# Performance work log

Hardware: AMD Instinct MI355X
Metric: run time of the kernel (lower is better)

Reference implementation:

```python
import jax, jax.numpy as jnp
import numpy as np

NUM_HEADS = 12


def setup_inputs() -> dict:
    key = jax.random.key(0)
    k1, k2, k3 = jax.random.split(key, 3)
    B, S, E = 1, 4096, 768
    x = jax.random.normal(k1, (B, S, E), dtype=jnp.float32)
    # learned parameters (nn.Linear weights, stored as [in, out] for x @ W)
    w_qkv = jax.random.normal(k2, (E, 3 * E), dtype=jnp.float32) * 0.02
    b_qkv = jnp.zeros((3 * E,), dtype=jnp.float32)
    w_out = jax.random.normal(k3, (E, E), dtype=jnp.float32) * 0.02
    b_out = jnp.zeros((E,), dtype=jnp.float32)
    return {"x": x, "w_qkv": w_qkv, "b_qkv": b_qkv, "w_out": w_out, "b_out": b_out}


def reference(x, w_qkv, b_qkv, w_out, b_out):
    """Single-process (world_size==1) path of the module:
    qkv projection -> multi-head scaled-dot-product softmax attention
    (non-causal) -> output projection. Dropout is identity in eval.
    """
    B, S, E = x.shape
    H = NUM_HEADS
    D = E // H
    scale = 1.0 / jnp.sqrt(jnp.asarray(D, dtype=x.dtype))

    qkv = x @ w_qkv + b_qkv                       # [B, S, 3E]
    qkv = qkv.reshape(B, S, 3, H, D)
    qkv = jnp.transpose(qkv, (2, 0, 3, 1, 4))     # [3, B, H, S, D]
    q, k, v = qkv[0], qkv[1], qkv[2]

    scores = jnp.einsum("bhqd,bhkd->bhqk", q * scale, k)  # [B, H, S, S]
    attn = jax.nn.softmax(scores, axis=-1)
    out = jnp.einsum("bhqk,bhkd->bhqd", attn, v)           # [B, H, S, D]

    out = jnp.transpose(out, (0, 2, 1, 3)).reshape(B, S, E)
    return out @ w_out + b_out
```

## Files before the change

kernel.cpp:

```cpp
#include <hip/hip_runtime.h>

typedef __attribute__((ext_vector_type(8))) short bh8;
typedef __attribute__((ext_vector_type(4))) float fx4;

__device__ __forceinline__ unsigned short f2bf(float f) {
    unsigned int u = __float_as_uint(f);
    u += 0x7FFF + ((u >> 16) & 1);
    return (unsigned short)(u >> 16);
}

__device__ __forceinline__ unsigned int cvtpk_bf16(float a, float b) {
    unsigned int r;
    asm("v_cvt_pk_bf16_f32 %0, %1, %2" : "=v"(r) : "v"(a), "v"(b));
    return r;
}

__device__ __forceinline__ bh8 pack4(unsigned int a, unsigned int b,
                                     unsigned int c, unsigned int d) {
    union { unsigned int u[4]; bh8 h; } z;
    z.u[0] = a; z.u[1] = b; z.u[2] = c; z.u[3] = d;
    return z.h;
}

__device__ __forceinline__ void stage_rows8(const unsigned short* g, long ldg,
                                            unsigned short* lds, int lane) {
    int r8 = lane >> 3;
    int gc = (lane & 7) ^ r8;
    __builtin_amdgcn_global_load_lds(
        (const __attribute__((address_space(1))) void*)(g + (long)r8 * ldg + gc * 8),
        (__attribute__((address_space(3))) void*)lds, 16, 0, 0);
}

__device__ __forceinline__ bh8 frag_ld(const unsigned short* t, int row, int kchunk, int lane) {
    int ch = (kchunk + (lane >> 4)) ^ (row & 7);
    return *(const bh8*)(t + row * 64 + ch * 8);
}

__global__ __launch_bounds__(256) void castbf(const float* __restrict__ x,
                                              unsigned short* __restrict__ y, int n) {
    int i = (blockIdx.x * 256 + threadIdx.x) * 4;
    if (i < n) {
        float4 v = *(const float4*)(x + i);
        ushort4 o = make_ushort4(f2bf(v.x), f2bf(v.y), f2bf(v.z), f2bf(v.w));
        *(ushort4*)(y + i) = o;
    }
}

__global__ __launch_bounds__(256) void transW(const float* __restrict__ W,
                                              unsigned short* __restrict__ Wt,
                                              int K, int N) {
    __shared__ float t[32][33];
    const int n0 = blockIdx.x * 32, k0 = blockIdx.y * 32;
    const int tx = threadIdx.x & 31, ty = threadIdx.x >> 5;
    #pragma unroll
    for (int r = ty; r < 32; r += 8)
        t[r][tx] = W[(size_t)(k0 + r) * N + n0 + tx];
    __syncthreads();
    #pragma unroll
    for (int r = ty; r < 32; r += 8)
        Wt[(size_t)(n0 + r) * K + k0 + tx] = f2bf(t[tx][r]);
}

__global__ __launch_bounds__(256) void gemm_qkv(const unsigned short* __restrict__ A,
                                                const unsigned short* __restrict__ Bt,
                                                const float* __restrict__ bias,
                                                unsigned short* __restrict__ Cout,
                                                unsigned short* __restrict__ vt) {
    const int M = 4096, N = 2304, K = 768;
    __shared__ __align__(16) char smem[49152];
    unsigned short* Ash0 = (unsigned short*)smem;
    unsigned short* Ash1 = (unsigned short*)(smem + 8192);
    unsigned short* Bsh0 = (unsigned short*)(smem + 16384);
    unsigned short* Bsh1 = (unsigned short*)(smem + 32768);
    unsigned short* Tsc  = (unsigned short*)smem;

    const int m0 = blockIdx.y * 64, n0 = blockIdx.x * 128;
    const int tid = threadIdx.x, wid = tid >> 6, lane = tid & 63;
    const int wr = (wid >> 1) * 32, wc = (wid & 1) * 64;

    #pragma unroll
    for (int g = 0; g < 2; ++g) {
        int rt = (wid * 2 + g) * 8;
        stage_rows8(A + (size_t)(m0 + rt) * K, K, Ash0 + rt * 64, lane);
    }
    #pragma unroll
    for (int g = 0; g < 4; ++g) {
        int rt = (wid * 4 + g) * 8;
        stage_rows8(Bt + (size_t)(n0 + rt) * K, K, Bsh0 + rt * 64, lane);
    }
    __syncthreads();

    fx4 acc[2][4];
    #pragma unroll
    for (int i = 0; i < 2; ++i)
        #pragma unroll
        for (int j = 0; j < 4; ++j)
            acc[i][j] = (fx4){0.f, 0.f, 0.f, 0.f};

    int kn = 64;
    auto kstep = [&](const unsigned short* Ac, const unsigned short* Bc,
                     unsigned short* Ad, unsigned short* Bd, bool pref) {
        if (pref) {
            #pragma unroll
            for (int g = 0; g < 2; ++g) {
                int rt = (wid * 2 + g) * 8;
                stage_rows8(A + (size_t)(m0 + rt) * K + kn, K, Ad + rt * 64, lane);
            }
            #pragma unroll
            for (int g = 0; g < 4; ++g) {
                int rt = (wid * 4 + g) * 8;
                stage_rows8(Bt + (size_t)(n0 + rt) * K + kn, K, Bd + rt * 64, lane);
            }
            kn += 64;
        }
        #pragma unroll
        for (int ks = 0; ks < 2; ++ks) {
            bh8 af[2], bfr[4];
            #pragma unroll
            for (int i = 0; i < 2; ++i) af[i] = frag_ld(Ac, wr + i * 16 + (lane & 15), ks * 4, lane);
            #pragma unroll
            for (int j = 0; j < 4; ++j) bfr[j] = frag_ld(Bc, wc + j * 16 + (lane & 15), ks * 4, lane);
            #pragma unroll
            for (int i = 0; i < 2; ++i)
                #pragma unroll
                for (int j = 0; j < 4; ++j)
                    acc[i][j] = __builtin_amdgcn_mfma_f32_16x16x32_bf16(af[i], bfr[j], acc[i][j], 0, 0, 0);
        }
        __syncthreads();
    };

    for (int t2 = 0; t2 < 6; ++t2) {
        kstep(Ash0, Bsh0, Ash1, Bsh1, true);
        kstep(Ash1, Bsh1, Ash0, Bsh0, t2 < 5);
    }

    const int cc = lane & 15, g4 = (lane >> 4) * 4;
    if (n0 < 1536) {
        #pragma unroll
        for (int j = 0; j < 4; ++j) {
            int col = n0 + wc + j * 16 + cc;
            float bv = bias[col];
            float sc = (col < 768) ? 0.18033688011112042f : 1.0f;
            #pragma unroll
            for (int i = 0; i < 2; ++i) {
                #pragma unroll
                for (int r = 0; r < 4; ++r) {
                    int row = m0 + wr + i * 16 + g4 + r;
                    Cout[(size_t)row * N + col] = f2bf((acc[i][j][r] + bv) * sc);
                }
            }
        }
    } else {
        #pragma unroll
        for (int j = 0; j < 4; ++j) {
            int dloc = wc + j * 16 + cc;
            float bv = bias[n0 + dloc];
            #pragma unroll
            for (int i = 0; i < 2; ++i) {
                int sloc = wr + i * 16 + g4;
                unsigned int u0 = cvtpk_bf16(acc[i][j][0] + bv, acc[i][j][1] + bv);
                unsigned int u1 = cvtpk_bf16(acc[i][j][2] + bv, acc[i][j][3] + bv);
                *(uint2*)(Tsc + dloc * 68 + sloc) = make_uint2(u0, u1);
            }
        }
        __syncthreads();
        const int d = tid >> 1, hf = (tid & 1) << 5;
        const unsigned short* srow = Tsc + d * 68;
        unsigned short* dst = vt + (size_t)(n0 - 1536 + d) * 4096 + m0 + hf;
        #pragma unroll
        for (int k = 0; k < 4; ++k) {
            int y = hf + 8 * k;
            int sb = (y & 32) + ((y & 24) >> 1);
            uint2 lo = *(const uint2*)(srow + sb);
            uint2 hi = *(const uint2*)(srow + sb + 16);
            *(uint4*)(dst + 8 * k) = make_uint4(lo.x, lo.y, hi.x, hi.y);
        }
    }
}

__global__ __launch_bounds__(256) void gemm64(const unsigned short* __restrict__ A,
                                              const unsigned short* __restrict__ Bt,
                                              const float* __restrict__ bias,
                                              float* __restrict__ Cout,
                                              int M, int N, int K) {
    __shared__ __align__(16) unsigned short Ash[2][64 * 64];
    __shared__ __align__(16) unsigned short Bsh[2][64 * 64];
    const int m0 = blockIdx.y * 64, n0 = blockIdx.x * 64;
    const int tid = threadIdx.x, wid = tid >> 6, lane = tid & 63;
    const int wr = (wid >> 1) * 32, wc = (wid & 1) * 32;

    #pragma unroll
    for (int g = 0; g < 2; ++g) {
        int rt = (wid * 2 + g) * 8;
        stage_rows8(A + (size_t)(m0 + rt) * K, K, Ash[0] + rt * 64, lane);
        stage_rows8(Bt + (size_t)(n0 + rt) * K, K, Bsh[0] + rt * 64, lane);
    }
    __syncthreads();

    fx4 acc[2][2];
    #pragma unroll
    for (int i = 0; i < 2; ++i)
        #pragma unroll
        for (int j = 0; j < 2; ++j)
            acc[i][j] = (fx4){0.f, 0.f, 0.f, 0.f};

    int kn = 64;
    auto kstep = [&](const unsigned short* Ac, const unsigned short* Bc,
                     unsigned short* Ad, unsigned short* Bd, bool pref) {
        if (pref) {
            #pragma unroll
            for (int g = 0; g < 2; ++g) {
                int rt = (wid * 2 + g) * 8;
                stage_rows8(A + (size_t)(m0 + rt) * K + kn, K, Ad + rt * 64, lane);
                stage_rows8(Bt + (size_t)(n0 + rt) * K + kn, K, Bd + rt * 64, lane);
            }
            kn += 64;
        }
        #pragma unroll
        for (int ks = 0; ks < 2; ++ks) {
            bh8 af[2], bfr[2];
            #pragma unroll
            for (int i = 0; i < 2; ++i) af[i] = frag_ld(Ac, wr + i * 16 + (lane & 15), ks * 4, lane);
            #pragma unroll
            for (int j = 0; j < 2; ++j) bfr[j] = frag_ld(Bc, wc + j * 16 + (lane & 15), ks * 4, lane);
            #pragma unroll
            for (int i = 0; i < 2; ++i)
                #pragma unroll
                for (int j = 0; j < 2; ++j)
                    acc[i][j] = __builtin_amdgcn_mfma_f32_16x16x32_bf16(af[i], bfr[j], acc[i][j], 0, 0, 0);
        }
        __syncthreads();
    };

    for (int t2 = 0; t2 < 6; ++t2) {
        kstep(Ash[0], Bsh[0], Ash[1], Bsh[1], true);
        kstep(Ash[1], Bsh[1], Ash[0], Bsh[0], t2 < 5);
    }

    const int cc = lane & 15, g4 = (lane >> 4) * 4;
    #pragma unroll
    for (int j = 0; j < 2; ++j) {
        int col = n0 + wc + j * 16 + cc;
        float bv = bias[col];
        #pragma unroll
        for (int i = 0; i < 2; ++i) {
            #pragma unroll
            for (int r = 0; r < 4; ++r) {
                int row = m0 + wr + i * 16 + g4 + r;
                Cout[(size_t)row * N + col] = acc[i][j][r] + bv;
            }
        }
    }
}

__global__ __launch_bounds__(256) void attn_fwd(const unsigned short* __restrict__ qkv,
                                                const unsigned short* __restrict__ vt,
                                                unsigned short* __restrict__ ao) {
    __shared__ __align__(16) char smem[40960];
    unsigned short* Qs  = (unsigned short*)smem;
    unsigned short* Ks0 = (unsigned short*)(smem + 8192);
    unsigned short* Ks1 = (unsigned short*)(smem + 16384);
    unsigned short* Vs0 = (unsigned short*)(smem + 24576);
    unsigned short* Vs1 = (unsigned short*)(smem + 32768);
    float* Of    = (float*)smem;
    float* l_lds = (float*)(smem + 17408);

    const int h = blockIdx.y, q0 = blockIdx.x * 64;
    const int tid = threadIdx.x, wid = tid >> 6, lane = tid & 63;
    const int g = lane >> 4, qc = lane & 15, x = qc & 7;
    const int wq = wid >> 1, wk = wid & 1;

    const unsigned short* qg_ = qkv + (size_t)q0 * 2304 + h * 64;
    const unsigned short* kgb = qkv + 768 + h * 64;
    const unsigned short* vgb = vt + (size_t)h * 64 * 4096;

    #pragma unroll
    for (int gg = 0; gg < 2; ++gg) {
        int rt = (wid * 2 + gg) * 8;
        stage_rows8(qg_ + (size_t)rt * 2304, 2304, Qs + rt * 64, lane);
        stage_rows8(kgb + (size_t)rt * 2304, 2304, Ks0 + rt * 64, lane);
        stage_rows8(vgb + (size_t)rt * 4096, 4096, Vs0 + rt * 64, lane);
    }
    __syncthreads();

    bh8 qf[2][2];
    #pragma unroll
    for (int qg = 0; qg < 2; ++qg)
        #pragma unroll
        for (int kc = 0; kc < 2; ++kc)
            qf[qg][kc] = frag_ld(Qs, 32 * wq + 16 * qg + qc, 4 * kc, lane);

    int koff[2][2], voff[4];
    #pragma unroll
    for (int jm = 0; jm < 2; ++jm)
        #pragma unroll
        for (int kc = 0; kc < 2; ++kc)
            koff[jm][kc] = (32 * wk + 16 * jm + qc) * 64 + ((4 * kc + g) ^ x) * 8;
    #pragma unroll
    for (int dj = 0; dj < 4; ++dj)
        voff[dj] = (16 * dj + qc) * 64 + ((4 * wk + g) ^ x) * 8;

    float lrun[2] = {0.f, 0.f};
    fx4 oacP[4][2];
    #pragma unroll
    for (int dj = 0; dj < 4; ++dj)
        #pragma unroll
        for (int qg = 0; qg < 2; ++qg)
            oacP[dj][qg] = (fx4){0.f, 0.f, 0.f, 0.f};

    const unsigned short* knext = kgb + (size_t)64 * 2304;
    const unsigned short* vnext = vgb + 64;

    auto tile_step = [&](const unsigned short* Kc, const unsigned short* Vc,
                         unsigned short* Kd, unsigned short* Vd, bool pref) {
        if (pref) {
            #pragma unroll
            for (int gg = 0; gg < 2; ++gg) {
                int rt = (wid * 2 + gg) * 8;
                stage_rows8(knext + (size_t)rt * 2304, 2304, Kd + rt * 64, lane);
                stage_rows8(vnext + (size_t)rt * 4096, 4096, Vd + rt * 64, lane);
            }
            knext += (size_t)64 * 2304;
            vnext += 64;
        }

        bh8 kf[2][2];
        #pragma unroll
        for (int jm = 0; jm < 2; ++jm) {
            kf[jm][0] = *(const bh8*)(Kc + koff[jm][0]);
            kf[jm][1] = *(const bh8*)(Kc + koff[jm][1]);
        }
        fx4 sT[2][2];
        __builtin_amdgcn_s_setprio(1);
        #pragma unroll
        for (int jm = 0; jm < 2; ++jm)
            #pragma unroll
            for (int qg = 0; qg < 2; ++qg) {
                fx4 z = (fx4){0.f, 0.f, 0.f, 0.f};
                z = __builtin_amdgcn_mfma_f32_16x16x32_bf16(kf[jm][0], qf[qg][0], z, 0, 0, 0);
                z = __builtin_amdgcn_mfma_f32_16x16x32_bf16(kf[jm][1], qf[qg][1], z, 0, 0, 0);
                sT[jm][qg] = z;
            }
        __builtin_amdgcn_s_setprio(0);

        #pragma unroll
        for (int jm = 0; jm < 2; ++jm)
            #pragma unroll
            for (int qg = 0; qg < 2; ++qg) {
                sT[jm][qg][0] = __builtin_amdgcn_exp2f(sT[jm][qg][0]);
                sT[jm][qg][1] = __builtin_amdgcn_exp2f(sT[jm][qg][1]);
                sT[jm][qg][2] = __builtin_amdgcn_exp2f(sT[jm][qg][2]);
                sT[jm][qg][3] = __builtin_amdgcn_exp2f(sT[jm][qg][3]);
                lrun[qg] += (sT[jm][qg][0] + sT[jm][qg][1]) + (sT[jm][qg][2] + sT[jm][qg][3]);
            }

        bh8 vf[4];
        #pragma unroll
        for (int dj = 0; dj < 4; ++dj) vf[dj] = *(const bh8*)(Vc + voff[dj]);
        __builtin_amdgcn_s_setprio(1);
        #pragma unroll
        for (int qg = 0; qg < 2; ++qg) {
            bh8 pb = pack4(cvtpk_bf16(sT[0][qg][0], sT[0][qg][1]),
                           cvtpk_bf16(sT[0][qg][2], sT[0][qg][3]),
                           cvtpk_bf16(sT[1][qg][0], sT[1][qg][1]),
                           cvtpk_bf16(sT[1][qg][2], sT[1][qg][3]));
            #pragma unroll
            for (int dj = 0; dj < 4; ++dj)
                oacP[dj][qg] = __builtin_amdgcn_mfma_f32_16x16x32_bf16(vf[dj], pb, oacP[dj][qg], 0, 0, 0);
        }
        __builtin_amdgcn_s_setprio(0);
        __syncthreads();
    };

    for (int t2 = 0; t2 < 32; ++t2) {
        tile_step(Ks0, Vs0, Ks1, Vs1, true);
        tile_step(Ks1, Vs1, Ks0, Vs0, t2 < 31);
    }

    #pragma unroll
    for (int qg = 0; qg < 2; ++qg) {
        lrun[qg] += __shfl_xor(lrun[qg], 16);
        lrun[qg] += __shfl_xor(lrun[qg], 32);
    }
    if (wk == 1) {
        #pragma unroll
        for (int qg = 0; qg < 2; ++qg) {
            int q = 32 * wq + 16 * qg + qc;
            #pragma unroll
            for (int dj = 0; dj < 4; ++dj)
                *(fx4*)(Of + q * 68 + 16 * dj + 4 * g) = oacP[dj][qg];
            l_lds[q] = lrun[qg];
        }
    }
    __syncthreads();
    if (wk == 0) {
        #pragma unroll
        for (int qg = 0; qg < 2; ++qg) {
            int q = 32 * wq + 16 * qg + qc;
            float inv = 1.0f / (lrun[qg] + l_lds[q]);
            unsigned short* aop = ao + (size_t)(q0 + q) * 768 + h * 64;
            #pragma unroll
            for (int dj = 0; dj < 4; ++dj) {
                fx4 o = oacP[dj][qg];
                fx4 p = *(const fx4*)(Of + q * 68 + 16 * dj + 4 * g);
                int d0 = dj * 16 + 4 * g;
                *(unsigned int*)(aop + d0)     = cvtpk_bf16((o[0] + p[0]) * inv, (o[1] + p[1]) * inv);
                *(unsigned int*)(aop + d0 + 2) = cvtpk_bf16((o[2] + p[2]) * inv, (o[3] + p[3]) * inv);
            }
        }
    }
}

extern "C" void kernel_launch(void* const* d_in, const int* in_sizes, int n_in,
                              void* d_out, int out_size, void* d_ws, size_t ws_size,
                              hipStream_t stream) {
    const float* x     = (const float*)d_in[0];
    const float* w_qkv = (const float*)d_in[1];
    const float* b_qkv = (const float*)d_in[2];
    const float* w_out = (const float*)d_in[3];
    const float* b_out = (const float*)d_in[4];
    float* out = (float*)d_out;

    const int S = 4096, E = 768, E3 = 2304, H = 12;

    unsigned short* xb    = (unsigned short*)d_ws;
    unsigned short* wqkvT = xb    + (size_t)S * E;
    unsigned short* woutT = wqkvT + (size_t)E3 * E;
    unsigned short* qkvb  = woutT + (size_t)E * E;
    unsigned short* vtp   = qkvb  + (size_t)S * E3;
    unsigned short* ao    = vtp   + (size_t)H * 64 * S;

    castbf<<<dim3((S * E) / (256 * 4)), 256, 0, stream>>>(x, xb, S * E);
    transW<<<dim3(E3 / 32, E / 32), 256, 0, stream>>>(w_qkv, wqkvT, E, E3);
    transW<<<dim3(E / 32, E / 32), 256, 0, stream>>>(w_out, woutT, E, E);
    gemm_qkv<<<dim3(E3 / 128, S / 64), 256, 0, stream>>>(xb, wqkvT, b_qkv, qkvb, vtp);
    attn_fwd<<<dim3(S / 64, H), 256, 0, stream>>>(qkvb, vtp, ao);
    gemm64<<<dim3(E / 64, S / 64), 256, 0, stream>>>(ao, woutT, b_out, out, S, E, E);
}
```

Before: 119.2 us.

## Enlarge QKV GEMM tile to 128x128 with swizzled block order and fuse prep kernels

Merges the cast of x to bf16 and both weight transposes into a single prep launch, removing two kernel launches. The QKV projection GEMM grows its tile from 64x128 to 128x128 (each wave now holds 4x4 MFMA accumulators) and uses a 1-D grid with a swizzled block-to-tile mapping for better L2 reuse. The V-transpose epilogue is adjusted to the larger tile. The larger tile raises register and LDS use (64 KB) and halves the block count to 576, which may lower occupancy.

```diff
diff --git a/kernel.cpp b/kernel.cpp
--- a/kernel.cpp
+++ b/kernel.cpp
@@ -36,21 +36,25 @@
     return *(const bh8*)(t + row * 64 + ch * 8);
 }
 
-__global__ __launch_bounds__(256) void castbf(const float* __restrict__ x,
-                                              unsigned short* __restrict__ y, int n) {
-    int i = (blockIdx.x * 256 + threadIdx.x) * 4;
-    if (i < n) {
+__global__ __launch_bounds__(256) void prep(const float* __restrict__ x,
+                                            unsigned short* __restrict__ xb,
+                                            const float* __restrict__ w_qkv,
+                                            unsigned short* __restrict__ wqkvT,
+                                            const float* __restrict__ w_out,
+                                            unsigned short* __restrict__ woutT) {
+    __shared__ float t[32][33];
+    const int bid = blockIdx.x;
+    if (bid < 3072) {
+        int i = (bid * 256 + threadIdx.x) * 4;
         float4 v = *(const float4*)(x + i);
-        ushort4 o = make_ushort4(f2bf(v.x), f2bf(v.y), f2bf(v.z), f2bf(v.w));
-        *(ushort4*)(y + i) = o;
-    }
-}
-
-__global__ __launch_bounds__(256) void transW(const float* __restrict__ W,
-                                              unsigned short* __restrict__ Wt,
-                                              int K, int N) {
-    __shared__ float t[32][33];
-    const int n0 = blockIdx.x * 32, k0 = blockIdx.y * 32;
+        *(ushort4*)(xb + i) = make_ushort4(f2bf(v.x), f2bf(v.y), f2bf(v.z), f2bf(v.w));
+        return;
+    }
+    const float* W; unsigned short* Wt; int N, xid;
+    if (bid < 3072 + 1728) { W = w_qkv; Wt = wqkvT; N = 2304; xid = bid - 3072; }
+    else                   { W = w_out; Wt = woutT; N = 768;  xid = bid - 4800; }
+    const int K = 768, nb = N / 32;
+    const int n0 = (xid % nb) * 32, k0 = (xid / nb) * 32;
     const int tx = threadIdx.x & 31, ty = threadIdx.x >> 5;
     #pragma unroll
     for (int r = ty; r < 32; r += 8)
@@ -66,33 +70,31 @@
                                                 const float* __restrict__ bias,
                                                 unsigned short* __restrict__ Cout,
                                                 unsigned short* __restrict__ vt) {
-    const int M = 4096, N = 2304, K = 768;
-    __shared__ __align__(16) char smem[49152];
+    const int N = 2304, K = 768;
+    __shared__ __align__(16) char smem[65536];
     unsigned short* Ash0 = (unsigned short*)smem;
-    unsigned short* Ash1 = (unsigned short*)(smem + 8192);
-    unsigned short* Bsh0 = (unsigned short*)(smem + 16384);
-    unsigned short* Bsh1 = (unsigned short*)(smem + 32768);
+    unsigned short* Ash1 = (unsigned short*)(smem + 16384);
+    unsigned short* Bsh0 = (unsigned short*)(smem + 32768);
+    unsigned short* Bsh1 = (unsigned short*)(smem + 49152);
     unsigned short* Tsc  = (unsigned short*)smem;
 
-    const int m0 = blockIdx.y * 64, n0 = blockIdx.x * 128;
+    const int bid = blockIdx.x;
+    const int swz = (bid & 7) * 72 + (bid >> 3);
+    const int m0 = (swz / 18) * 128, n0 = (swz % 18) * 128;
     const int tid = threadIdx.x, wid = tid >> 6, lane = tid & 63;
-    const int wr = (wid >> 1) * 32, wc = (wid & 1) * 64;
-
-    #pragma unroll
-    for (int g = 0; g < 2; ++g) {
-        int rt = (wid * 2 + g) * 8;
-        stage_rows8(A + (size_t)(m0 + rt) * K, K, Ash0 + rt * 64, lane);
-    }
+    const int wr = (wid >> 1) * 64, wc = (wid & 1) * 64;
+
     #pragma unroll
     for (int g = 0; g < 4; ++g) {
         int rt = (wid * 4 + g) * 8;
+        stage_rows8(A + (size_t)(m0 + rt) * K, K, Ash0 + rt * 64, lane);
         stage_rows8(Bt + (size_t)(n0 + rt) * K, K, Bsh0 + rt * 64, lane);
     }
     __syncthreads();
 
-    fx4 acc[2][4];
-    #pragma unroll
-    for (int i = 0; i < 2; ++i)
+    fx4 acc[4][4];
+    #pragma unroll
+    for (int i = 0; i < 4; ++i)
         #pragma unroll
         for (int j = 0; j < 4; ++j)
             acc[i][j] = (fx4){0.f, 0.f, 0.f, 0.f};
@@ -102,26 +104,22 @@
                      unsigned short* Ad, unsigned short* Bd, bool pref) {
         if (pref) {
             #pragma unroll
-            for (int g = 0; g < 2; ++g) {
-                int rt = (wid * 2 + g) * 8;
-                stage_rows8(A + (size_t)(m0 + rt) * K + kn, K, Ad + rt * 64, lane);
-            }
-            #pragma unroll
             for (int g = 0; g < 4; ++g) {
                 int rt = (wid * 4 + g) * 8;
+                stage_rows8(A + (size_t)(m0 + rt) * K + kn, K, Ad + rt * 64, lane);
                 stage_rows8(Bt + (size_t)(n0 + rt) * K + kn, K, Bd + rt * 64, lane);
             }
             kn += 64;
         }
         #pragma unroll
         for (int ks = 0; ks < 2; ++ks) {
-            bh8 af[2], bfr[4];
-            #pragma unroll
-            for (int i = 0; i < 2; ++i) af[i] = frag_ld(Ac, wr + i * 16 + (lane & 15), ks * 4, lane);
+            bh8 af[4], bfr[4];
+            #pragma unroll
+            for (int i = 0; i < 4; ++i) af[i] = frag_ld(Ac, wr + i * 16 + (lane & 15), ks * 4, lane);
             #pragma unroll
             for (int j = 0; j < 4; ++j) bfr[j] = frag_ld(Bc, wc + j * 16 + (lane & 15), ks * 4, lane);
             #pragma unroll
-            for (int i = 0; i < 2; ++i)
+            for (int i = 0; i < 4; ++i)
                 #pragma unroll
                 for (int j = 0; j < 4; ++j)
                     acc[i][j] = __builtin_amdgcn_mfma_f32_16x16x32_bf16(af[i], bfr[j], acc[i][j], 0, 0, 0);
@@ -142,7 +140,7 @@
             float bv = bias[col];
             float sc = (col < 768) ? 0.18033688011112042f : 1.0f;
             #pragma unroll
-            for (int i = 0; i < 2; ++i) {
+            for (int i = 0; i < 4; ++i) {
                 #pragma unroll
                 for (int r = 0; r < 4; ++r) {
                     int row = m0 + wr + i * 16 + g4 + r;
@@ -156,20 +154,20 @@
             int dloc = wc + j * 16 + cc;
             float bv = bias[n0 + dloc];
             #pragma unroll
-            for (int i = 0; i < 2; ++i) {
+            for (int i = 0; i < 4; ++i) {
                 int sloc = wr + i * 16 + g4;
                 unsigned int u0 = cvtpk_bf16(acc[i][j][0] + bv, acc[i][j][1] + bv);
                 unsigned int u1 = cvtpk_bf16(acc[i][j][2] + bv, acc[i][j][3] + bv);
-                *(uint2*)(Tsc + dloc * 68 + sloc) = make_uint2(u0, u1);
+                *(uint2*)(Tsc + dloc * 132 + sloc) = make_uint2(u0, u1);
             }
         }
         __syncthreads();
-        const int d = tid >> 1, hf = (tid & 1) << 5;
-        const unsigned short* srow = Tsc + d * 68;
-        unsigned short* dst = vt + (size_t)(n0 - 1536 + d) * 4096 + m0 + hf;
-        #pragma unroll
-        for (int k = 0; k < 4; ++k) {
-            int y = hf + 8 * k;
+        const int d = tid >> 1, bblk = tid & 1;
+        const unsigned short* srow = Tsc + d * 132 + bblk * 64;
+        unsigned short* dst = vt + (size_t)(n0 - 1536 + d) * 4096 + m0 + bblk * 64;
+        #pragma unroll
+        for (int k = 0; k < 8; ++k) {
+            int y = 8 * k;
             int sb = (y & 32) + ((y & 24) >> 1);
             uint2 lo = *(const uint2*)(srow + sb);
             uint2 hi = *(const uint2*)(srow + sb + 16);
@@ -430,10 +428,8 @@
     unsigned short* vtp   = qkvb  + (size_t)S * E3;
     unsigned short* ao    = vtp   + (size_t)H * 64 * S;
 
-    castbf<<<dim3((S * E) / (256 * 4)), 256, 0, stream>>>(x, xb, S * E);
-    transW<<<dim3(E3 / 32, E / 32), 256, 0, stream>>>(w_qkv, wqkvT, E, E3);
-    transW<<<dim3(E / 32, E / 32), 256, 0, stream>>>(w_out, woutT, E, E);
-    gemm_qkv<<<dim3(E3 / 128, S / 64), 256, 0, stream>>>(xb, wqkvT, b_qkv, qkvb, vtp);
+    prep<<<dim3(3072 + 1728 + 576), 256, 0, stream>>>(x, xb, w_qkv, wqkvT, w_out, woutT);
+    gemm_qkv<<<dim3(576), 256, 0, stream>>>(xb, wqkvT, b_qkv, qkvb, vtp);
     attn_fwd<<<dim3(S / 64, H), 256, 0, stream>>>(qkvb, vtp, ao);
     gemm64<<<dim3(E / 64, S / 64), 256, 0, stream>>>(ao, woutT, b_out, out, S, E, E);
 }
```

New measurement: 116.9 us. About the same (-1.9%).
